# Optimization experiments

Hardware: AMD Instinct MI355X
Metric: run time of the kernel (lower is better)

Reference implementation:

```python
import math
import jax, jax.numpy as jnp
import numpy as np

T, C, NE = 4096, 2048, 2048
LAYER_ID, NUM_LAYERS = 12, 24


def setup_inputs() -> dict:
    key = jax.random.key(0)
    ks = jax.random.split(key, 5)
    r01 = LAYER_ID / (NUM_LAYERS - 1)
    r1a0 = 1.0 - LAYER_ID / NUM_LAYERS
    idx = jnp.arange(C, dtype=jnp.float32)
    # parameter inits faithful to the haiku module
    time_decay = -5.0 + 8.0 * (idx / (C - 1)) ** (0.7 + 1.3 * r01)
    time_first = jnp.full((C,), math.log(0.3), jnp.float32) + (jnp.mod(idx + 1, 3) - 1.0) * 0.5
    ddd = (idx / C)[None, :]  # [1, C]
    time_mix_k = jnp.power(ddd, r1a0)
    time_mix_v = jnp.power(ddd, r1a0) + 0.3 * r01
    time_mix_r = jnp.power(ddd, r1a0 * 0.5)
    scale = 0.02  # ~ 1/sqrt(fan_in), keeps exp(k) stable
    x = jax.random.normal(ks[0], (T, NE), jnp.float32)
    Wk = jax.random.normal(ks[1], (NE, C), jnp.float32) * scale
    Wv = jax.random.normal(ks[2], (NE, C), jnp.float32) * scale
    Wr = jax.random.normal(ks[3], (NE, C), jnp.float32) * scale
    Wo = jax.random.normal(ks[4], (C, NE), jnp.float32) * scale
    return {"x": x, "time_first": time_first, "time_decay": time_decay,
            "time_mix_k": time_mix_k, "time_mix_v": time_mix_v, "time_mix_r": time_mix_r,
            "Wk": Wk, "Wv": Wv, "Wr": Wr, "Wo": Wo}


def wkv_conv(w, u, k, v):
    # w,u: [C]; k,v: [T,C].  Faithful conv-trick WKV from the source module.
    w = -jnp.exp(w)
    kT, vT = k.T, v.T                      # [C, T]
    ek = jnp.exp(kT)
    a = ek * vT
    Tlen = kT.shape[1]
    Cn = kT.shape[0]
    # depthwise conv kernel: exp(decay * relative position), last tap = exp(u)
    td = jnp.arange(-(Tlen - 2), 1, dtype=kT.dtype)[None, :] * jnp.exp(w)[:, None]  # [C, T-1]
    td = jnp.concatenate([td, u[:, None]], axis=1)                                   # [C, T]
    kernel = jnp.exp(td)[:, None]           # [C, 1, T]
    a3 = jnp.pad(a[None], ((0, 0), (0, 0), (Tlen - 1, 0)))   # [1, C, 2T-1]
    k3 = jnp.pad(ek[None], ((0, 0), (0, 0), (Tlen - 1, 0)))
    num = jax.lax.conv_general_dilated(a3, kernel, (1,), [(0, 0)], feature_group_count=Cn)
    den = jax.lax.conv_general_dilated(k3, kernel, (1,), [(0, 0)], feature_group_count=Cn)
    return (num / den)[0]                   # [C, T]


def reference(x, time_first, time_decay, time_mix_k, time_mix_v, time_mix_r, Wk, Wv, Wr, Wo):
    xx = jnp.pad(x, ((1, 0), (0, 0)))[:-1]          # time shift
    xk = x * time_mix_k + xx * (1.0 - time_mix_k)
    xv = x * time_mix_v + xx * (1.0 - time_mix_v)
    xr = x * time_mix_r + xx * (1.0 - time_mix_r)
    k = xk @ Wk                                     # [T, C]
    v = xv @ Wv
    r = xr @ Wr
    sr = jax.nn.sigmoid(r)
    wkv = wkv_conv(time_decay, time_first, k, v).T  # [T, C]
    return (sr * wkv) @ Wo                          # [T, n_embd]
```

## Files before the change

kernel.cpp:

```cpp
#include <hip/hip_runtime.h>
#include <hip/hip_bf16.h>
#include <cstdint>
#include <cstddef>

#define T_LEN   4096
#define C_DIM   2048
#define NE_DIM  2048
#define CHUNK   64
#define NCHUNK  (T_LEN / CHUNK)

typedef __bf16 bf16;
typedef __attribute__((ext_vector_type(8))) __bf16 bf16x8;
typedef __attribute__((ext_vector_type(4))) __bf16 bf16x4;
typedef __attribute__((ext_vector_type(4))) float  f32x4;

__device__ __forceinline__ void gld_lds16(bf16* lds_dst, const bf16* g_src) {
  __builtin_amdgcn_global_load_lds(
      (__attribute__((address_space(1))) void*)(g_src),
      (__attribute__((address_space(3))) void*)(lds_dst),
      16, 0, 0);
}

__global__ __launch_bounds__(256) void mix_kernel(
    const float* __restrict__ x,
    const float* __restrict__ tmk, const float* __restrict__ tmv,
    const float* __restrict__ tmr,
    bf16* __restrict__ xk, bf16* __restrict__ xv, bf16* __restrict__ xr)
{
  int gid = blockIdx.x * 256 + threadIdx.x;
  int row = gid / (NE_DIM / 4);
  int e4  = gid % (NE_DIM / 4);
  const f32x4* x4 = (const f32x4*)x;
  f32x4 zero = {0.f, 0.f, 0.f, 0.f};
  f32x4 xc = x4[gid];
  f32x4 xp = (row > 0) ? x4[gid - NE_DIM / 4] : zero;
  f32x4 mk = ((const f32x4*)tmk)[e4];
  f32x4 mv = ((const f32x4*)tmv)[e4];
  f32x4 mr = ((const f32x4*)tmr)[e4];
  f32x4 vk = xc * mk + xp * (1.0f - mk);
  f32x4 vv = xc * mv + xp * (1.0f - mv);
  f32x4 vr = xc * mr + xp * (1.0f - mr);
  bf16x4 ok, ov, orr;
#pragma unroll
  for (int i = 0; i < 4; ++i) {
    ok[i]  = (bf16)vk[i];
    ov[i]  = (bf16)vv[i];
    orr[i] = (bf16)vr[i];
  }
  *(bf16x4*)(xk + (size_t)gid * 4) = ok;
  *(bf16x4*)(xv + (size_t)gid * 4) = ov;
  *(bf16x4*)(xr + (size_t)gid * 4) = orr;
}

__global__ __launch_bounds__(256) void wtrans(
    const float* __restrict__ W0, const float* __restrict__ W1,
    const float* __restrict__ W2, const float* __restrict__ W3,
    bf16* __restrict__ O0, bf16* __restrict__ O1,
    bf16* __restrict__ O2, bf16* __restrict__ O3)
{
  __shared__ float tile[32][33];
  int z = blockIdx.z;
  const float* W = (z == 0) ? W0 : (z == 1) ? W1 : (z == 2) ? W2 : W3;
  bf16* O        = (z == 0) ? O0 : (z == 1) ? O1 : (z == 2) ? O2 : O3;
  int bx = blockIdx.x * 32, by = blockIdx.y * 32;
  int tx = threadIdx.x, ty = threadIdx.y;
#pragma unroll
  for (int j = 0; j < 4; ++j)
    tile[ty + j * 8][tx] = W[(size_t)(by + ty + j * 8) * NE_DIM + bx + tx];
  __syncthreads();
#pragma unroll
  for (int j = 0; j < 4; ++j)
    O[(size_t)(bx + ty + j * 8) * NE_DIM + by + tx] = (bf16)tile[tx][ty + j * 8];
}

#define BM 128
#define BN 128
#define BK 32
__global__ __launch_bounds__(256) void gemm_bt(
    const bf16* __restrict__ A, const bf16* __restrict__ Bt,
    float* __restrict__ C, int M, int N, int K)
{
  __shared__ __align__(16) bf16 As[BM * BK];
  __shared__ __align__(16) bf16 Bs[BN * BK];
  int tid = threadIdx.x;
  int bm = blockIdx.y, bn = blockIdx.x;
  int w = tid >> 6, lane = tid & 63;
  int wm = w >> 1, wn = w & 1;
  int lr = lane & 15, kb = lane >> 4;
  f32x4 acc[4][4] = {};

  const bf16* Ab = A  + (size_t)(bm * BM) * K;
  const bf16* Bb = Bt + (size_t)(bn * BN) * K;
  int s0 = tid, s1 = tid + 256;
  int r0 = s0 >> 2, c0 = (s0 & 3) * 8;
  int r1 = s1 >> 2, c1 = (s1 & 3) * 8;

  for (int k0 = 0; k0 < K; k0 += BK) {
    gld_lds16(&As[s0 * 8], Ab + (size_t)r0 * K + k0 + c0);
    gld_lds16(&As[s1 * 8], Ab + (size_t)r1 * K + k0 + c1);
    gld_lds16(&Bs[s0 * 8], Bb + (size_t)r0 * K + k0 + c0);
    gld_lds16(&Bs[s1 * 8], Bb + (size_t)r1 * K + k0 + c1);
    __syncthreads();

    bf16x8 af[4], bfr[4];
#pragma unroll
    for (int mi = 0; mi < 4; ++mi)
      af[mi] = *(const bf16x8*)&As[(wm * 64 + mi * 16 + lr) * BK + kb * 8];
#pragma unroll
    for (int ni = 0; ni < 4; ++ni)
      bfr[ni] = *(const bf16x8*)&Bs[(wn * 64 + ni * 16 + lr) * BK + kb * 8];
#pragma unroll
    for (int mi = 0; mi < 4; ++mi)
#pragma unroll
      for (int ni = 0; ni < 4; ++ni)
        acc[mi][ni] = __builtin_amdgcn_mfma_f32_16x16x32_bf16(
            af[mi], bfr[ni], acc[mi][ni], 0, 0, 0);
    __syncthreads();
  }

#pragma unroll
  for (int mi = 0; mi < 4; ++mi)
#pragma unroll
    for (int ni = 0; ni < 4; ++ni) {
      int rbase = bm * BM + wm * 64 + mi * 16 + kb * 4;
      int col   = bn * BN + wn * 64 + ni * 16 + lr;
#pragma unroll
      for (int j = 0; j < 4; ++j)
        C[(size_t)(rbase + j) * N + col] = acc[mi][ni][j];
    }
}

__global__ __launch_bounds__(256) void wkv_phase1(
    const float* __restrict__ k, const float* __restrict__ v,
    const float* __restrict__ td,
    float* __restrict__ SA, float* __restrict__ SB)
{
  int c = blockIdx.x * 256 + threadIdx.x;
  int m = blockIdx.y;
  float f = __expf(-__expf(td[c]));
  float D = __expf(-f);
  float sa = 0.f, sb = 0.f;
  size_t base = (size_t)m * CHUNK * C_DIM + c;
  for (int t = 0; t < CHUNK; ++t) {
    float ek = __expf(k[base + (size_t)t * C_DIM]);
    float vv = v[base + (size_t)t * C_DIM];
    sa = D * sa + ek * vv;
    sb = D * sb + ek;
  }
  SA[(size_t)m * C_DIM + c] = sa;
  SB[(size_t)m * C_DIM + c] = sb;
}

__global__ __launch_bounds__(256) void wkv_phase2(
    const float* __restrict__ td,
    const float* __restrict__ SA, const float* __restrict__ SB,
    float* __restrict__ A0, float* __restrict__ B0)
{
  int c = blockIdx.x * 256 + threadIdx.x;
  float f  = __expf(-__expf(td[c]));
  float DL = __expf(-f * (float)CHUNK);
  float a = 0.f, b = 0.f;
  for (int m = 0; m < NCHUNK; ++m) {
    A0[(size_t)m * C_DIM + c] = a;
    B0[(size_t)m * C_DIM + c] = b;
    a = DL * a + SA[(size_t)m * C_DIM + c];
    b = DL * b + SB[(size_t)m * C_DIM + c];
  }
}

__global__ __launch_bounds__(256) void wkv_phase3(
    const float* __restrict__ k, const float* __restrict__ v,
    const float* __restrict__ r,
    const float* __restrict__ td, const float* __restrict__ tf,
    const float* __restrict__ A0, const float* __restrict__ B0,
    bf16* __restrict__ y)
{
  int c = blockIdx.x * 256 + threadIdx.x;
  int m = blockIdx.y;
  float f  = __expf(-__expf(td[c]));
  float D  = __expf(-f);
  float eu = __expf(tf[c]);
  float a = A0[(size_t)m * C_DIM + c];
  float b = B0[(size_t)m * C_DIM + c];
  size_t base = (size_t)m * CHUNK * C_DIM + c;
  for (int t = 0; t < CHUNK; ++t) {
    size_t idx = base + (size_t)t * C_DIM;
    float kk = k[idx], vv = v[idx], rr = r[idx];
    float ek  = __expf(kk);
    float euk = eu * ek;
    float wkv = (a + euk * vv) / (b + euk);
    float sr  = 1.0f / (1.0f + __expf(-rr));
    y[idx] = (bf16)(sr * wkv);
    a = D * a + ek * vv;
    b = D * b + ek;
  }
}

extern "C" void kernel_launch(void* const* d_in, const int* in_sizes, int n_in,
                              void* d_out, int out_size, void* d_ws, size_t ws_size,
                              hipStream_t stream)
{
  (void)in_sizes; (void)n_in; (void)out_size; (void)ws_size;
  const float* x   = (const float*)d_in[0];
  const float* tf  = (const float*)d_in[1];
  const float* td  = (const float*)d_in[2];
  const float* tmk = (const float*)d_in[3];
  const float* tmv = (const float*)d_in[4];
  const float* tmr = (const float*)d_in[5];
  const float* Wk  = (const float*)d_in[6];
  const float* Wv  = (const float*)d_in[7];
  const float* Wr  = (const float*)d_in[8];
  const float* Wo  = (const float*)d_in[9];
  float* out = (float*)d_out;

  char* ws = (char*)d_ws;
  size_t off = 0;
  auto alloc = [&](size_t bytes) {
    void* p = ws + off;
    off += (bytes + 255) & ~(size_t)255;
    return p;
  };
  const size_t TN  = (size_t)T_LEN * NE_DIM;
  const size_t WN  = (size_t)C_DIM * NE_DIM;

  bf16* xk  = (bf16*)alloc(TN * 2);
  bf16* xv  = (bf16*)alloc(TN * 2);
  bf16* xr  = (bf16*)alloc(TN * 2);
  bf16* WkT = (bf16*)alloc(WN * 2);
  bf16* WvT = (bf16*)alloc(WN * 2);
  bf16* WrT = (bf16*)alloc(WN * 2);
  bf16* WoT = (bf16*)alloc(WN * 2);
  float* kb = (float*)alloc(TN * 4);
  float* vb = (float*)alloc(TN * 4);
  float* rb = (float*)alloc(TN * 4);
  bf16*  y  = xk;
  float* SA = (float*)xv;
  float* SB = SA + (size_t)NCHUNK * C_DIM;
  float* A0 = SB + (size_t)NCHUNK * C_DIM;
  float* B0 = A0 + (size_t)NCHUNK * C_DIM;

  mix_kernel<<<dim3((unsigned)(TN / 4 / 256)), 256, 0, stream>>>(
      x, tmk, tmv, tmr, xk, xv, xr);
  wtrans<<<dim3(64, 64, 4), dim3(32, 8), 0, stream>>>(
      Wk, Wv, Wr, Wo, WkT, WvT, WrT, WoT);
  dim3 ggrid(NE_DIM / BN, T_LEN / BM);
  gemm_bt<<<ggrid, 256, 0, stream>>>(xk, WkT, kb, T_LEN, C_DIM, NE_DIM);
  gemm_bt<<<ggrid, 256, 0, stream>>>(xv, WvT, vb, T_LEN, C_DIM, NE_DIM);
  gemm_bt<<<ggrid, 256, 0, stream>>>(xr, WrT, rb, T_LEN, C_DIM, NE_DIM);
  wkv_phase1<<<dim3(C_DIM / 256, NCHUNK), 256, 0, stream>>>(kb, vb, td, SA, SB);
  wkv_phase2<<<dim3(C_DIM / 256), 256, 0, stream>>>(td, SA, SB, A0, B0);
  wkv_phase3<<<dim3(C_DIM / 256, NCHUNK), 256, 0, stream>>>(
      kb, vb, rb, td, tf, A0, B0, y);
  gemm_bt<<<ggrid, 256, 0, stream>>>(y, WoT, out, T_LEN, NE_DIM, C_DIM);
}
```

Baseline: 437.8 us.

## Replace GEMM with 8-wave 128x256 double-buffered pipelined MFMA kernel

Replaces the simple single-buffered 128x128 BK=32 GEMM with a 512-thread kernel using 128x256 tiles and BK=64. LDS is double-buffered with an XOR swizzle, and async global-to-LDS loads are interleaved with MFMA quadrants under manual barriers and vmcnt waits. It also adds a block-index swizzle for L2 locality and raises MFMA priority with setprio. The goal is to hide load latency and cut per-tile synchronization overhead. The kernel hardcodes K=2048 and the output stride, and its fragile hand-written schedule risks races.

```diff
diff --git a/kernel.cpp b/kernel.cpp
--- a/kernel.cpp
+++ b/kernel.cpp
@@ -73,60 +73,119 @@
     O[(size_t)(bx + ty + j * 8) * NE_DIM + by + tx] = (bf16)tile[tx][ty + j * 8];
 }
 
-#define BM 128
-#define BN 128
-#define BK 32
-__global__ __launch_bounds__(256) void gemm_bt(
+#define GK 2048
+#define NTILE (GK / 64)
+#define NITER (NTILE / 2)
+
+#define BARS() asm volatile("s_barrier" ::: "memory")
+#define VMC(n) asm volatile("s_waitcnt vmcnt(" #n ")" ::: "memory")
+
+#define STAGE_A(b, h, kt) \
+  gld_lds16(&sm[(b)*8192 + ((h)*512 + tid)*8], \
+            Abase + (size_t)((h)*64 + sr) * GK + (kt)*64)
+#define STAGE_B(b, h, kt) do { \
+  gld_lds16(&sm[16384 + (b)*16384 + ((h)*1024 + tid)*8], \
+            Bbase + (size_t)((h)*128 + sr) * GK + (kt)*64); \
+  gld_lds16(&sm[16384 + (b)*16384 + ((h)*1024 + 512 + tid)*8], \
+            Bbase + (size_t)((h)*128 + 64 + sr) * GK + (kt)*64); \
+} while (0)
+
+#define LDA(b, fr, kh) (*(const bf16x8*)&sm[(b)*8192 + rA##fr * 64 + colx##kh * 8])
+#define LDB(b, fc, kh) (*(const bf16x8*)&sm[16384 + (b)*16384 + rB##fc * 64 + colx##kh * 8])
+
+#define RDA01(b) do { af[0][0]=LDA(b,0,0); af[0][1]=LDA(b,0,1); \
+                      af[1][0]=LDA(b,1,0); af[1][1]=LDA(b,1,1); } while(0)
+#define RDA23(b) do { af[2][0]=LDA(b,2,0); af[2][1]=LDA(b,2,1); \
+                      af[3][0]=LDA(b,3,0); af[3][1]=LDA(b,3,1); } while(0)
+#define RDB01(b) do { bfr[0][0]=LDB(b,0,0); bfr[0][1]=LDB(b,0,1); \
+                      bfr[1][0]=LDB(b,1,0); bfr[1][1]=LDB(b,1,1); } while(0)
+#define RDB23(b) do { bfr[2][0]=LDB(b,2,0); bfr[2][1]=LDB(b,2,1); \
+                      bfr[3][0]=LDB(b,3,0); bfr[3][1]=LDB(b,3,1); } while(0)
+
+#define MFMA1(F, G) do { \
+  acc[F][G] = __builtin_amdgcn_mfma_f32_16x16x32_bf16(af[F][0], bfr[G][0], acc[F][G], 0,0,0); \
+  acc[F][G] = __builtin_amdgcn_mfma_f32_16x16x32_bf16(af[F][1], bfr[G][1], acc[F][G], 0,0,0); \
+} while (0)
+#define MQ(F, G) do { __builtin_amdgcn_s_setprio(1); \
+  MFMA1(F,G); MFMA1(F,(G)+1); MFMA1((F)+1,G); MFMA1((F)+1,(G)+1); \
+  __builtin_amdgcn_s_setprio(0); } while (0)
+
+__global__ __launch_bounds__(512, 2) void gemm8(
     const bf16* __restrict__ A, const bf16* __restrict__ Bt,
-    float* __restrict__ C, int M, int N, int K)
-{
-  __shared__ __align__(16) bf16 As[BM * BK];
-  __shared__ __align__(16) bf16 Bs[BN * BK];
-  int tid = threadIdx.x;
-  int bm = blockIdx.y, bn = blockIdx.x;
-  int w = tid >> 6, lane = tid & 63;
-  int wm = w >> 1, wn = w & 1;
-  int lr = lane & 15, kb = lane >> 4;
+    float* __restrict__ C)
+{
+  __shared__ __align__(16) bf16 sm[49152];
+  const int tid  = threadIdx.x;
+  const int lane = tid & 63, w = tid >> 6;
+  const int wm = w >> 2, wn = w & 3;
+  const int lr = lane & 15, kb = lane >> 4;
+
+  int wg  = blockIdx.x;
+  int swz = (wg & 7) * 32 + (wg >> 3);
+  int bn  = swz >> 5, bm = swz & 31;
+
+  const int sr = tid >> 3;
+  const int sc = (tid & 7) ^ (sr & 7);
+  const bf16* Abase = A  + (size_t)(bm * 128) * GK + sc * 8;
+  const bf16* Bbase = Bt + (size_t)(bn * 256) * GK + sc * 8;
+
+  const int colx0 = kb ^ (lr & 7);
+  const int colx1 = colx0 ^ 4;
+  const int rA0 = wm * 32 + lr,        rA1 = rA0 + 16;
+  const int rA2 = 64 + wm * 32 + lr,   rA3 = rA2 + 16;
+  const int rB0 = wn * 32 + lr,        rB1 = rB0 + 16;
+  const int rB2 = 128 + wn * 32 + lr,  rB3 = rB2 + 16;
+
   f32x4 acc[4][4] = {};
-
-  const bf16* Ab = A  + (size_t)(bm * BM) * K;
-  const bf16* Bb = Bt + (size_t)(bn * BN) * K;
-  int s0 = tid, s1 = tid + 256;
-  int r0 = s0 >> 2, c0 = (s0 & 3) * 8;
-  int r1 = s1 >> 2, c1 = (s1 & 3) * 8;
-
-  for (int k0 = 0; k0 < K; k0 += BK) {
-    gld_lds16(&As[s0 * 8], Ab + (size_t)r0 * K + k0 + c0);
-    gld_lds16(&As[s1 * 8], Ab + (size_t)r1 * K + k0 + c1);
-    gld_lds16(&Bs[s0 * 8], Bb + (size_t)r0 * K + k0 + c0);
-    gld_lds16(&Bs[s1 * 8], Bb + (size_t)r1 * K + k0 + c1);
-    __syncthreads();
-
-    bf16x8 af[4], bfr[4];
-#pragma unroll
-    for (int mi = 0; mi < 4; ++mi)
-      af[mi] = *(const bf16x8*)&As[(wm * 64 + mi * 16 + lr) * BK + kb * 8];
-#pragma unroll
-    for (int ni = 0; ni < 4; ++ni)
-      bfr[ni] = *(const bf16x8*)&Bs[(wn * 64 + ni * 16 + lr) * BK + kb * 8];
-#pragma unroll
-    for (int mi = 0; mi < 4; ++mi)
-#pragma unroll
-      for (int ni = 0; ni < 4; ++ni)
-        acc[mi][ni] = __builtin_amdgcn_mfma_f32_16x16x32_bf16(
-            af[mi], bfr[ni], acc[mi][ni], 0, 0, 0);
-    __syncthreads();
-  }
-
-#pragma unroll
-  for (int mi = 0; mi < 4; ++mi)
-#pragma unroll
-    for (int ni = 0; ni < 4; ++ni) {
-      int rbase = bm * BM + wm * 64 + mi * 16 + kb * 4;
-      int col   = bn * BN + wn * 64 + ni * 16 + lr;
+  bf16x8 af[4][2], bfr[4][2];
+
+  STAGE_A(0, 0, 0); STAGE_A(0, 1, 0); STAGE_B(0, 0, 0); STAGE_B(0, 1, 0);
+  STAGE_B(1, 0, 1); STAGE_A(1, 1, 1);
+  VMC(3); BARS();
+
+  for (int i = 0; i < NITER - 1; ++i) {
+    const int t1 = 2 * i + 1, t2 = 2 * i + 2, t3 = 2 * i + 3;
+    RDA01(0); RDB01(0); STAGE_A(1, 0, t1);
+    BARS(); MQ(0, 0); BARS();
+    RDA23(0); STAGE_B(1, 1, t1);
+    BARS(); MQ(2, 0); BARS();
+    RDB23(0); STAGE_B(0, 0, t2);
+    BARS(); MQ(2, 2); BARS();
+    STAGE_A(0, 1, t2);
+    VMC(3); BARS(); MQ(0, 2); BARS();
+    RDA01(1); RDB01(1); STAGE_A(0, 0, t2);
+    BARS(); MQ(0, 0); BARS();
+    RDA23(1); STAGE_B(0, 1, t2);
+    BARS(); MQ(2, 0); BARS();
+    RDB23(1); STAGE_B(1, 0, t3);
+    BARS(); MQ(2, 2); BARS();
+    STAGE_A(1, 1, t3);
+    VMC(3); BARS(); MQ(0, 2); BARS();
+  }
+  RDA01(0); RDB01(0); STAGE_A(1, 0, NTILE - 1);
+  BARS(); MQ(0, 0); BARS();
+  RDA23(0); STAGE_B(1, 1, NTILE - 1);
+  BARS(); MQ(2, 0); BARS();
+  RDB23(0);
+  BARS(); MQ(2, 2); BARS();
+  VMC(0); BARS(); MQ(0, 2); BARS();
+  RDA01(1); RDB01(1);
+  BARS(); MQ(0, 0); BARS();
+  RDA23(1);
+  BARS(); MQ(2, 0); BARS();
+  RDB23(1);
+  BARS(); MQ(2, 2); BARS();
+  MQ(0, 2);
+
+#pragma unroll
+  for (int fr = 0; fr < 4; ++fr)
+#pragma unroll
+    for (int fc = 0; fc < 4; ++fc) {
+      size_t r0 = (size_t)(bm * 128) + (fr >> 1) * 64 + wm * 32 + (fr & 1) * 16 + kb * 4;
+      int    c0 = bn * 256 + (fc >> 1) * 128 + wn * 32 + (fc & 1) * 16 + lr;
 #pragma unroll
       for (int j = 0; j < 4; ++j)
-        C[(size_t)(rbase + j) * N + col] = acc[mi][ni][j];
+        C[(r0 + j) * C_DIM + c0] = acc[fr][fc][j];
     }
 }
 
@@ -243,13 +302,12 @@
       x, tmk, tmv, tmr, xk, xv, xr);
   wtrans<<<dim3(64, 64, 4), dim3(32, 8), 0, stream>>>(
       Wk, Wv, Wr, Wo, WkT, WvT, WrT, WoT);
-  dim3 ggrid(NE_DIM / BN, T_LEN / BM);
-  gemm_bt<<<ggrid, 256, 0, stream>>>(xk, WkT, kb, T_LEN, C_DIM, NE_DIM);
-  gemm_bt<<<ggrid, 256, 0, stream>>>(xv, WvT, vb, T_LEN, C_DIM, NE_DIM);
-  gemm_bt<<<ggrid, 256, 0, stream>>>(xr, WrT, rb, T_LEN, C_DIM, NE_DIM);
+  gemm8<<<dim3(256), 512, 0, stream>>>(xk, WkT, kb);
+  gemm8<<<dim3(256), 512, 0, stream>>>(xv, WvT, vb);
+  gemm8<<<dim3(256), 512, 0, stream>>>(xr, WrT, rb);
   wkv_phase1<<<dim3(C_DIM / 256, NCHUNK), 256, 0, stream>>>(kb, vb, td, SA, SB);
   wkv_phase2<<<dim3(C_DIM / 256), 256, 0, stream>>>(td, SA, SB, A0, B0);
   wkv_phase3<<<dim3(C_DIM / 256, NCHUNK), 256, 0, stream>>>(
       kb, vb, rb, td, tf, A0, B0, y);
-  gemm_bt<<<ggrid, 256, 0, stream>>>(y, WoT, out, T_LEN, NE_DIM, C_DIM);
-}
+  gemm8<<<dim3(256), 512, 0, stream>>>(y, WoT, out);
+}
```

Result: faster. 371.4 us (-15.2%).
